# Optimization experiments

Measured on AMD Instinct MI355X. Metric: run time of the kernel, lower is better.

## Reference

```python
import jax, jax.numpy as jnp
import numpy as np

N, F_IN, F_OUT, K = 4096, 32, 32, 2
NEG_SLOPE = 0.2
MASK_VAL = -9e15


def _sparse_mat(kv, km, density=0.01):
    vals = jax.random.normal(kv, (N, N), dtype=jnp.float32)
    mask = jax.random.uniform(km, (N, N)) < density
    return vals * mask


def setup_inputs() -> dict:
    key = jax.random.key(0)
    ks = jax.random.split(key, 12)
    x = jax.random.normal(ks[0], (N, F_IN), dtype=jnp.float32)
    Ld = _sparse_mat(ks[1], ks[2])
    Lu = _sparse_mat(ks[3], ks[4])
    P = jax.random.normal(ks[5], (N, N), dtype=jnp.float32) / np.sqrt(N)
    W1 = jax.random.normal(ks[6], (K, F_IN, F_OUT), dtype=jnp.float32) * 0.1
    W2 = jax.random.normal(ks[7], (K, F_IN, F_OUT), dtype=jnp.float32) * 0.1
    W0 = jax.random.normal(ks[8], (F_IN, F_OUT), dtype=jnp.float32) * 0.1
    att1 = jax.random.normal(ks[9], (2 * F_OUT * K, 1), dtype=jnp.float32) * 0.1
    att2 = jax.random.normal(ks[10], (2 * F_OUT * K, 1), dtype=jnp.float32) * 0.1
    return {"x": x, "Ld": Ld, "Lu": Lu, "P": P, "W1": W1, "W2": W2,
            "W0": W0, "att1": att1, "att2": att2}


def _branch(x, L, W, att):
    # W: [K, F_in, F_out]; precompute x @ W[k] for all k -> [K, N, F_out]
    Kk, _, Fo = W.shape
    xw = jnp.einsum('nf,kfo->kno', x, W)
    # torch.cat([x@W[k]], dim=1) == transpose+reshape of xw
    xcat = jnp.transpose(xw, (1, 0, 2)).reshape(x.shape[0], Kk * Fo)
    d = Fo * Kk
    e = xcat @ att[:d] + (xcat @ att[d:]).T            # [N, N]
    e = jax.nn.leaky_relu(e, negative_slope=NEG_SLOPE)
    e = jnp.where(L != 0, e, MASK_VAL)
    alpha = jax.nn.softmax(e, axis=1)                   # row softmax, no dropout (eval)
    z = alpha @ xw[0]
    a = alpha
    for k in range(1, Kk):
        a = a @ L
        z = z + a @ xw[k]
    return z


def reference(x, Ld, Lu, P, W1, W2, W0, att1, att2):
    z1 = _branch(x, Ld, W1, att1)
    z2 = _branch(x, Lu, W2, att2)
    x0 = P @ (x @ W0)
    return z1 + z2 + x0
```

## Files before the change

kernel.cpp:

```cpp
#include <hip/hip_runtime.h>
#include <hip/hip_bf16.h>

#define NN 4096
#define CAP 128
#define KS 8

typedef __attribute__((ext_vector_type(8))) short bf16x8;
typedef __attribute__((ext_vector_type(4))) float f32x4;

__device__ __forceinline__ float lrelu(float v) { return v >= 0.f ? v : 0.2f * v; }

__device__ __forceinline__ ushort f2bu(float f) {
    unsigned u = __float_as_uint(f);
    return (ushort)((u + 0x7FFFu + ((u >> 16) & 1u)) >> 16);
}

__global__ __launch_bounds__(256) void k_prep(
    const float* __restrict__ x,
    const float* __restrict__ W1, const float* __restrict__ W2,
    const float* __restrict__ W0,
    const float* __restrict__ att1, const float* __restrict__ att2,
    float* __restrict__ xwA1, float* __restrict__ xwB1,
    float* __restrict__ xwA2, float* __restrict__ xwB2,
    float* __restrict__ a1, float* __restrict__ b1,
    float* __restrict__ a2, float* __restrict__ b2,
    __hip_bfloat16* __restrict__ Bt)
{
    __shared__ float wl[5120];
    __shared__ float xs[256];
    const int t = threadIdx.x;
    for (int i = t; i < 2048; i += 256) { wl[i] = W1[i]; wl[2048 + i] = W2[i]; }
    for (int i = t; i < 1024; i += 256) wl[4096 + i] = W0[i];
    const int rowBase = blockIdx.x * 8;
    xs[t] = x[rowBase * 32 + t];
    __syncthreads();

    const int o = t & 31, r = t >> 5;
    const int row = rowBase + r;
    const float* xr = &xs[r * 32];
    float vA1 = 0.f, vB1 = 0.f, vA2 = 0.f, vB2 = 0.f, v0 = 0.f;
#pragma unroll
    for (int f = 0; f < 32; ++f) {
        const float xv = xr[f];
        vA1 += xv * wl[f * 32 + o];
        vB1 += xv * wl[1024 + f * 32 + o];
        vA2 += xv * wl[2048 + f * 32 + o];
        vB2 += xv * wl[3072 + f * 32 + o];
        v0  += xv * wl[4096 + f * 32 + o];
    }
    xwA1[row * 32 + o] = vA1;
    xwB1[row * 32 + o] = vB1;
    xwA2[row * 32 + o] = vA2;
    xwB2[row * 32 + o] = vB2;
    ((ushort*)Bt)[(size_t)o * NN + row] = f2bu(v0);

    float pa1 = vA1 * att1[o]      + vB1 * att1[32 + o];
    float pb1 = vA1 * att1[64 + o] + vB1 * att1[96 + o];
    float pa2 = vA2 * att2[o]      + vB2 * att2[32 + o];
    float pb2 = vA2 * att2[64 + o] + vB2 * att2[96 + o];
#pragma unroll
    for (int m = 1; m <= 16; m <<= 1) {
        pa1 += __shfl_xor(pa1, m); pb1 += __shfl_xor(pb1, m);
        pa2 += __shfl_xor(pa2, m); pb2 += __shfl_xor(pb2, m);
    }
    if (o == 0) { a1[row] = pa1; b1[row] = pb1; a2[row] = pa2; b2[row] = pb2; }
}

__global__ __launch_bounds__(256) void k_csr(
    const float* __restrict__ Ld, const float* __restrict__ Lu,
    int2* __restrict__ csrv, int* __restrict__ cntArr)
{
    const int row = blockIdx.x;
    const int t = threadIdx.x, lane = t & 63, w = t >> 6;
    __shared__ int wcnt[16];

    float4 v[8];
    const float4* A4 = (const float4*)(Ld + (size_t)row * NN);
    const float4* B4 = (const float4*)(Lu + (size_t)row * NN);
#pragma unroll
    for (int it = 0; it < 4; ++it) { v[it] = A4[it * 256 + t]; v[4 + it] = B4[it * 256 + t]; }

    const unsigned long long lt = (1ull << lane) - 1ull;
#pragma unroll
    for (int br = 0; br < 2; ++br) {
        int2* out = csrv + ((size_t)br * NN + row) * CAP;
        int tots[4];
#pragma unroll
        for (int it = 0; it < 4; ++it) {
            const float4 fv = v[br * 4 + it];
            tots[it] = __popcll(__ballot(fv.x != 0.f)) + __popcll(__ballot(fv.y != 0.f))
                     + __popcll(__ballot(fv.z != 0.f)) + __popcll(__ballot(fv.w != 0.f));
        }
        __syncthreads();
        if (lane == 0) {
            int4 tv; tv.x = tots[0]; tv.y = tots[1]; tv.z = tots[2]; tv.w = tots[3];
            *(int4*)&wcnt[w * 4] = tv;
        }
        __syncthreads();
        const int4 ca = *(const int4*)&wcnt[0];
        const int4 cb = *(const int4*)&wcnt[4];
        const int4 cc = *(const int4*)&wcnt[8];
        const int4 cd = *(const int4*)&wcnt[12];
        const int cs[16] = {ca.x, ca.y, ca.z, ca.w, cb.x, cb.y, cb.z, cb.w,
                            cc.x, cc.y, cc.z, cc.w, cd.x, cd.y, cd.z, cd.w};
        int total = 0;
#pragma unroll
        for (int k2 = 0; k2 < 16; ++k2) total += cs[k2];
        int base = 0;
#pragma unroll
        for (int k2 = 0; k2 < 16; ++k2) base += (k2 < (w << 2)) ? cs[k2] : 0;
        const int cnt  = min(total, CAP);
        const int cp16 = min((cnt + 15) & ~15, CAP);

#pragma unroll
        for (int it = 0; it < 4; ++it) {
            const float4 fv = v[br * 4 + it];
            const unsigned long long m0 = __ballot(fv.x != 0.f);
            const unsigned long long m1 = __ballot(fv.y != 0.f);
            const unsigned long long m2 = __ballot(fv.z != 0.f);
            const unsigned long long m3 = __ballot(fv.w != 0.f);
            const int p0 = __popcll(m0), p1 = __popcll(m1), p2 = __popcll(m2);
            const int c0 = (it * 256 + t) * 4;
            int s;
            s = base + __popcll(m0 & lt);
            if (fv.x != 0.f && s < CAP) { int2 e; e.x = c0;     e.y = __float_as_int(fv.x); out[s] = e; }
            s = base + p0 + __popcll(m1 & lt);
            if (fv.y != 0.f && s < CAP) { int2 e; e.x = c0 + 1; e.y = __float_as_int(fv.y); out[s] = e; }
            s = base + p0 + p1 + __popcll(m2 & lt);
            if (fv.z != 0.f && s < CAP) { int2 e; e.x = c0 + 2; e.y = __float_as_int(fv.z); out[s] = e; }
            s = base + p0 + p1 + p2 + __popcll(m3 & lt);
            if (fv.w != 0.f && s < CAP) { int2 e; e.x = c0 + 3; e.y = __float_as_int(fv.w); out[s] = e; }
            base += p0 + p1 + p2 + __popcll(m3);
        }
        if (t >= cnt && t < cp16) { int2 e; e.x = 0; e.y = 0; out[t] = e; }
        if (t == 0) cntArr[br * NN + row] = cnt;
    }
}

__global__ __launch_bounds__(256) void k_gather(
    const int2* __restrict__ csrv, const int* __restrict__ cntArr,
    const float* __restrict__ xwB1, const float* __restrict__ xwB2,
    const float* __restrict__ xwA1, const float* __restrict__ xwA2,
    float* __restrict__ u1, float* __restrict__ u2)
{
    __shared__ int2 sle[4][CAP];
    const int w = threadIdx.x >> 6, lane = threadIdx.x & 63;
    const int row = blockIdx.x * 4 + w;
    const int br  = blockIdx.y;
    const float* xwB = br ? xwB2 : xwB1;
    const float* xwA = br ? xwA2 : xwA1;
    float* u = br ? u2 : u1;

    const int cnt  = cntArr[br * NN + row];
    const int cp16 = min((cnt + 15) & ~15, CAP);
    const int2* ci = csrv + ((size_t)br * NN + row) * CAP;
    int2* se = sle[w];
    if (lane < cp16)      se[lane]      = ci[lane];
    if (lane + 64 < cp16) se[lane + 64] = ci[lane + 64];

    const int o = lane & 31, g = lane >> 5;
    float acc = 0.f;
    const int nb = cp16 >> 3;
    for (int j = 0; j < nb; ++j) {
        float wv[4], xv[4];
#pragma unroll
        for (int q = 0; q < 4; ++q) {
            const int2 e = se[8 * j + 2 * q + g];
            wv[q] = __int_as_float(e.y);
            xv[q] = xwB[(size_t)e.x * 32 + o];
        }
#pragma unroll
        for (int q = 0; q < 4; ++q) acc += wv[q] * xv[q];
    }
    acc += __shfl_xor(acc, 32);
    if (lane < 32) u[(size_t)row * 32 + o] = acc + xwA[(size_t)row * 32 + o];
}

__global__ __launch_bounds__(256) void k_attn(
    const int2* __restrict__ csrv, const int* __restrict__ cntArr,
    const float* __restrict__ a1, const float* __restrict__ b1,
    const float* __restrict__ a2, const float* __restrict__ b2,
    const float* __restrict__ u1, const float* __restrict__ u2,
    float* __restrict__ z1, float* __restrict__ z2)
{
    const int br = blockIdx.y;
    const int* cntB = cntArr + br * NN;
    const float* aA = br ? a2 : a1;
    const float* bA = br ? b2 : b1;
    const float* U  = br ? u2 : u1;
    float* z = br ? z2 : z1;

    __shared__ float sw[4 * CAP];
    __shared__ int   sci[4 * CAP];
    const int w = threadIdx.x >> 6, lane = threadIdx.x & 63;
    const int row = blockIdx.x * 4 + w;
    const int cnt = cntB[row];
    const int cp16 = min((cnt + 15) & ~15, CAP);
    const float ai = aA[row];
    const int2* ci = csrv + ((size_t)br * NN + row) * CAP;
    float* swg = sw + w * CAP;
    int*   scg = sci + w * CAP;

    int id0 = 0, id1 = 0;
    if (lane < cp16)      id0 = ci[lane].x;
    if (lane + 64 < cp16) id1 = ci[lane + 64].x;
    float e0 = (lane < cnt)      ? lrelu(ai + bA[id0]) : -1e30f;
    float e1 = (lane + 64 < cnt) ? lrelu(ai + bA[id1]) : -1e30f;
    float lmax = fmaxf(e0, e1);
#pragma unroll
    for (int m = 1; m <= 32; m <<= 1) lmax = fmaxf(lmax, __shfl_xor(lmax, m));
    const float w0 = __expf(e0 - lmax), w1 = __expf(e1 - lmax);
    float ssum = w0 + w1;
#pragma unroll
    for (int m = 1; m <= 32; m <<= 1) ssum += __shfl_xor(ssum, m);
    swg[lane] = w0; swg[lane + 64] = w1;
    scg[lane] = id0; scg[lane + 64] = id1;

    const int o = lane & 31, h = lane >> 5;
    float acc = 0.f;
    const int nb = cp16 >> 3;
    if (cnt > 0) {
        float wgA[4], uvA[4];
#pragma unroll
        for (int q = 0; q < 4; ++q) {
            const int s = h + 2 * q;
            wgA[q] = swg[s];
            uvA[q] = U[(size_t)scg[s] * 32 + o];
        }
        for (int j = 1; j < nb; ++j) {
            float wgB[4], uvB[4];
#pragma unroll
            for (int q = 0; q < 4; ++q) {
                const int s = h + 8 * j + 2 * q;
                wgB[q] = swg[s];
                uvB[q] = U[(size_t)scg[s] * 32 + o];
            }
#pragma unroll
            for (int q = 0; q < 4; ++q) acc += wgA[q] * uvA[q];
#pragma unroll
            for (int q = 0; q < 4; ++q) { wgA[q] = wgB[q]; uvA[q] = uvB[q]; }
        }
#pragma unroll
        for (int q = 0; q < 4; ++q) acc += wgA[q] * uvA[q];
    }
    acc += __shfl_xor(acc, 32);
    if (lane < 32) z[(size_t)row * 32 + o] = (cnt > 0) ? acc / ssum : 0.f;
}

__global__ __launch_bounds__(256) void k_pgemm(
    const float* __restrict__ P, const ushort* __restrict__ Bt,
    float* __restrict__ partial)
{
    __shared__ ushort sA[2][16 * 64 * 8];
    __shared__ ushort sB[2][8 * 64 * 8];
    const int t = threadIdx.x;
    const int row0 = blockIdx.x * 64;
    const int ks = blockIdx.y;
    const float4*  P4  = (const float4*)P;
    const ushort4* Bt4 = (const ushort4*)Bt;

    const int lane = t & 63, w = t >> 6;

    f32x4 acc0 = {0.f, 0.f, 0.f, 0.f};
    f32x4 acc1 = {0.f, 0.f, 0.f, 0.f};

    auto stageA = [&](int c, int buf) {
        const int kc4 = (ks * 512 + c * 128) >> 2;
#pragma unroll
        for (int j = 0; j < 8; ++j) {
            const int i = t + 256 * j;
            const int row = i >> 5, q = i & 31;
            const float4 v = P4[(size_t)(row0 + row) * 1024 + kc4 + q];
            ushort4 u;
            u.x = f2bu(v.x); u.y = f2bu(v.y); u.z = f2bu(v.z); u.w = f2bu(v.w);
            const int wi = row >> 4, m = row & 15;
            const int kk = q >> 3, quad = (q >> 1) & 3, jj = q & 1;
            *(ushort4*)&sA[buf][(((wi * 4 + kk) * 64) + quad * 16 + m) * 8 + jj * 4] = u;
        }
    };
    auto stageB = [&](int c, int buf) {
        const int kc4 = (ks * 512 + c * 128) >> 2;
#pragma unroll
        for (int j = 0; j < 4; ++j) {
            const int i = t + 256 * j;
            const int o = i >> 5, q = i & 31;
            const ushort4 u = Bt4[(size_t)o * 1024 + kc4 + q];
            const int nt = o >> 4, n = o & 15;
            const int kk = q >> 3, quad = (q >> 1) & 3, jj = q & 1;
            *(ushort4*)&sB[buf][(((kk * 2 + nt) * 64) + quad * 16 + n) * 8 + jj * 4] = u;
        }
    };
    auto compute = [&](int buf) {
        const ushort* pa = &sA[buf][(w * 4) * 64 * 8 + lane * 8];
        const ushort* pb = &sB[buf][lane * 8];
#pragma unroll
        for (int kk = 0; kk < 4; ++kk) {
            const bf16x8 a  = *(const bf16x8*)(pa + kk * 512);
            const bf16x8 b0 = *(const bf16x8*)(pb + kk * 1024);
            const bf16x8 b1 = *(const bf16x8*)(pb + kk * 1024 + 512);
            acc0 = __builtin_amdgcn_mfma_f32_16x16x32_bf16(a, b0, acc0, 0, 0, 0);
            acc1 = __builtin_amdgcn_mfma_f32_16x16x32_bf16(a, b1, acc1, 0, 0, 0);
        }
    };

    stageA(0, 0); stageB(0, 0);
    __syncthreads();
    for (int c = 0; c < 4; ++c) {
        if (c < 3) { stageA(c + 1, (c + 1) & 1); stageB(c + 1, (c + 1) & 1); }
        compute(c & 1);
        __syncthreads();
    }

    const int m = lane & 15, quad = lane >> 4;
    float* out = partial + ((size_t)ks * NN + row0 + w * 16 + quad * 4) * 32;
#pragma unroll
    for (int r = 0; r < 4; ++r) {
        out[r * 32 + m]      = acc0[r];
        out[r * 32 + 16 + m] = acc1[r];
    }
}

__global__ __launch_bounds__(256) void k_combine(
    const float4* __restrict__ z1, const float4* __restrict__ z2,
    const float4* __restrict__ partial, float4* __restrict__ out)
{
    const int i = blockIdx.x * 256 + threadIdx.x;
    const float4 a = z1[i], b = z2[i];
    float rx = a.x + b.x, ry = a.y + b.y, rz = a.z + b.z, rw = a.w + b.w;
#pragma unroll
    for (int p = 0; p < KS; ++p) {
        const float4 c = partial[p * 32768 + i];
        rx += c.x; ry += c.y; rz += c.z; rw += c.w;
    }
    float4 rr; rr.x = rx; rr.y = ry; rr.z = rz; rr.w = rw;
    out[i] = rr;
}

extern "C" void kernel_launch(void* const* d_in, const int* in_sizes, int n_in,
                              void* d_out, int out_size, void* d_ws, size_t ws_size,
                              hipStream_t stream) {
    (void)in_sizes; (void)n_in; (void)out_size; (void)ws_size;
    const float* x    = (const float*)d_in[0];
    const float* Ld   = (const float*)d_in[1];
    const float* Lu   = (const float*)d_in[2];
    const float* P    = (const float*)d_in[3];
    const float* W1   = (const float*)d_in[4];
    const float* W2   = (const float*)d_in[5];
    const float* W0   = (const float*)d_in[6];
    const float* att1 = (const float*)d_in[7];
    const float* att2 = (const float*)d_in[8];

    float* ws = (float*)d_ws;
    float* xwA1 = ws;
    float* xwB1 = ws + 131072;
    float* xwA2 = ws + 262144;
    float* xwB2 = ws + 393216;
    float* u1   = ws + 524288;
    float* u2   = ws + 655360;
    float* z1   = ws + 786432;
    float* z2   = ws + 917504;
    float* a1   = ws + 1048576;
    float* b1   = ws + 1052672;
    float* a2   = ws + 1056768;
    float* b2   = ws + 1060864;
    float* partial = ws + 1064960;
    __hip_bfloat16* Bt = (__hip_bfloat16*)(ws + 2113536);
    int2* csrv = (int2*)(ws + 2179072);
    int*  cnt  = (int*)(ws + 4276224);

    k_prep<<<512, 256, 0, stream>>>(x, W1, W2, W0, att1, att2,
                                    xwA1, xwB1, xwA2, xwB2, a1, b1, a2, b2, Bt);
    k_csr<<<NN, 256, 0, stream>>>(Ld, Lu, csrv, cnt);
    k_gather<<<dim3(NN / 4, 2), 256, 0, stream>>>(csrv, cnt, xwB1, xwB2,
                                                  xwA1, xwA2, u1, u2);
    k_attn<<<dim3(NN / 4, 2), 256, 0, stream>>>(csrv, cnt, a1, b1, a2, b2,
                                                u1, u2, z1, z2);
    k_pgemm<<<dim3(64, KS), 256, 0, stream>>>(P, (const ushort*)Bt, partial);
    k_combine<<<128, 256, 0, stream>>>((const float4*)z1, (const float4*)z2,
                                       (const float4*)partial, (float4*)d_out);
}
```

Baseline: 235.9 us.

## Co-schedule P GEMM with CSR build and fuse combine into attention

The dense P@(xW0) GEMM blocks are interleaved into the CSR-extraction kernel (every 9th block does GEMM work), so the compute-bound MFMA work overlaps with the bandwidth-bound scan of Ld/Lu. The attention kernel now handles both branches per row and also sums the split-K partials, writing the final output directly. This removes the separate pgemm and combine launches and the z1/z2 round-trips. In exchange, the GEMM loses its double-buffered LDS staging, and the fused kernel's shared memory footprint may reduce occupancy for the CSR blocks.

```diff
diff --git a/kernel.cpp b/kernel.cpp
--- a/kernel.cpp
+++ b/kernel.cpp
@@ -66,74 +66,134 @@
     if (o == 0) { a1[row] = pa1; b1[row] = pb1; a2[row] = pa2; b2[row] = pb2; }
 }
 
-__global__ __launch_bounds__(256) void k_csr(
+__global__ __launch_bounds__(256) void k_work(
     const float* __restrict__ Ld, const float* __restrict__ Lu,
-    int2* __restrict__ csrv, int* __restrict__ cntArr)
+    const float* __restrict__ P, const ushort* __restrict__ Bt,
+    int2* __restrict__ csrv, int* __restrict__ cntArr,
+    float* __restrict__ partial)
 {
-    const int row = blockIdx.x;
-    const int t = threadIdx.x, lane = t & 63, w = t >> 6;
-    __shared__ int wcnt[16];
-
-    float4 v[8];
-    const float4* A4 = (const float4*)(Ld + (size_t)row * NN);
-    const float4* B4 = (const float4*)(Lu + (size_t)row * NN);
-#pragma unroll
-    for (int it = 0; it < 4; ++it) { v[it] = A4[it * 256 + t]; v[4 + it] = B4[it * 256 + t]; }
-
-    const unsigned long long lt = (1ull << lane) - 1ull;
-#pragma unroll
-    for (int br = 0; br < 2; ++br) {
-        int2* out = csrv + ((size_t)br * NN + row) * CAP;
-        int tots[4];
-#pragma unroll
-        for (int it = 0; it < 4; ++it) {
-            const float4 fv = v[br * 4 + it];
-            tots[it] = __popcll(__ballot(fv.x != 0.f)) + __popcll(__ballot(fv.y != 0.f))
-                     + __popcll(__ballot(fv.z != 0.f)) + __popcll(__ballot(fv.w != 0.f));
-        }
-        __syncthreads();
-        if (lane == 0) {
-            int4 tv; tv.x = tots[0]; tv.y = tots[1]; tv.z = tots[2]; tv.w = tots[3];
-            *(int4*)&wcnt[w * 4] = tv;
-        }
-        __syncthreads();
-        const int4 ca = *(const int4*)&wcnt[0];
-        const int4 cb = *(const int4*)&wcnt[4];
-        const int4 cc = *(const int4*)&wcnt[8];
-        const int4 cd = *(const int4*)&wcnt[12];
-        const int cs[16] = {ca.x, ca.y, ca.z, ca.w, cb.x, cb.y, cb.z, cb.w,
-                            cc.x, cc.y, cc.z, cc.w, cd.x, cd.y, cd.z, cd.w};
-        int total = 0;
-#pragma unroll
-        for (int k2 = 0; k2 < 16; ++k2) total += cs[k2];
-        int base = 0;
-#pragma unroll
-        for (int k2 = 0; k2 < 16; ++k2) base += (k2 < (w << 2)) ? cs[k2] : 0;
-        const int cnt  = min(total, CAP);
-        const int cp16 = min((cnt + 15) & ~15, CAP);
-
-#pragma unroll
-        for (int it = 0; it < 4; ++it) {
-            const float4 fv = v[br * 4 + it];
-            const unsigned long long m0 = __ballot(fv.x != 0.f);
-            const unsigned long long m1 = __ballot(fv.y != 0.f);
-            const unsigned long long m2 = __ballot(fv.z != 0.f);
-            const unsigned long long m3 = __ballot(fv.w != 0.f);
-            const int p0 = __popcll(m0), p1 = __popcll(m1), p2 = __popcll(m2);
-            const int c0 = (it * 256 + t) * 4;
-            int s;
-            s = base + __popcll(m0 & lt);
-            if (fv.x != 0.f && s < CAP) { int2 e; e.x = c0;     e.y = __float_as_int(fv.x); out[s] = e; }
-            s = base + p0 + __popcll(m1 & lt);
-            if (fv.y != 0.f && s < CAP) { int2 e; e.x = c0 + 1; e.y = __float_as_int(fv.y); out[s] = e; }
-            s = base + p0 + p1 + __popcll(m2 & lt);
-            if (fv.z != 0.f && s < CAP) { int2 e; e.x = c0 + 2; e.y = __float_as_int(fv.z); out[s] = e; }
-            s = base + p0 + p1 + p2 + __popcll(m3 & lt);
-            if (fv.w != 0.f && s < CAP) { int2 e; e.x = c0 + 3; e.y = __float_as_int(fv.w); out[s] = e; }
-            base += p0 + p1 + p2 + __popcll(m3);
-        }
-        if (t >= cnt && t < cp16) { int2 e; e.x = 0; e.y = 0; out[t] = e; }
-        if (t == 0) cntArr[br * NN + row] = cnt;
+    __shared__ ushort sA[16 * 64 * 8];
+    __shared__ ushort sB[8 * 64 * 8];
+    const int t = threadIdx.x;
+    const int lane = t & 63, w = t >> 6;
+    const int bx = blockIdx.x;
+
+    if (bx % 9 == 0) {
+        const int bp = bx / 9;
+        const int row0 = (bp & 63) * 64;
+        const int ks = bp >> 6;
+        const float4*  P4  = (const float4*)P;
+        const ushort4* Bt4 = (const ushort4*)Bt;
+        f32x4 acc0 = {0.f, 0.f, 0.f, 0.f};
+        f32x4 acc1 = {0.f, 0.f, 0.f, 0.f};
+
+        for (int c = 0; c < 4; ++c) {
+            const int kc4 = (ks * 512 + c * 128) >> 2;
+#pragma unroll
+            for (int j = 0; j < 8; ++j) {
+                const int i = t + 256 * j;
+                const int row = i >> 5, q = i & 31;
+                const float4 v = P4[(size_t)(row0 + row) * 1024 + kc4 + q];
+                ushort4 u;
+                u.x = f2bu(v.x); u.y = f2bu(v.y); u.z = f2bu(v.z); u.w = f2bu(v.w);
+                const int wi = row >> 4, m = row & 15;
+                const int kk = q >> 3, quad = (q >> 1) & 3, jj = q & 1;
+                *(ushort4*)&sA[(((wi * 4 + kk) * 64) + quad * 16 + m) * 8 + jj * 4] = u;
+            }
+#pragma unroll
+            for (int j = 0; j < 4; ++j) {
+                const int i = t + 256 * j;
+                const int o = i >> 5, q = i & 31;
+                const ushort4 u = Bt4[(size_t)o * 1024 + kc4 + q];
+                const int nt = o >> 4, n = o & 15;
+                const int kk = q >> 3, quad = (q >> 1) & 3, jj = q & 1;
+                *(ushort4*)&sB[(((kk * 2 + nt) * 64) + quad * 16 + n) * 8 + jj * 4] = u;
+            }
+            __syncthreads();
+            const ushort* pa = &sA[(w * 4) * 64 * 8 + lane * 8];
+            const ushort* pb = &sB[lane * 8];
+#pragma unroll
+            for (int kk = 0; kk < 4; ++kk) {
+                const bf16x8 a  = *(const bf16x8*)(pa + kk * 512);
+                const bf16x8 b0 = *(const bf16x8*)(pb + kk * 1024);
+                const bf16x8 b1 = *(const bf16x8*)(pb + kk * 1024 + 512);
+                acc0 = __builtin_amdgcn_mfma_f32_16x16x32_bf16(a, b0, acc0, 0, 0, 0);
+                acc1 = __builtin_amdgcn_mfma_f32_16x16x32_bf16(a, b1, acc1, 0, 0, 0);
+            }
+            __syncthreads();
+        }
+        const int m = lane & 15, quad = lane >> 4;
+        float* out = partial + ((size_t)ks * NN + row0 + w * 16 + quad * 4) * 32;
+#pragma unroll
+        for (int r = 0; r < 4; ++r) {
+            out[r * 32 + m]      = acc0[r];
+            out[r * 32 + 16 + m] = acc1[r];
+        }
+    } else {
+        const int row = bx - 1 - bx / 9;
+        int* wcnt = (int*)sA;
+
+        float4 v[8];
+        const float4* A4 = (const float4*)(Ld + (size_t)row * NN);
+        const float4* B4 = (const float4*)(Lu + (size_t)row * NN);
+#pragma unroll
+        for (int it = 0; it < 4; ++it) { v[it] = A4[it * 256 + t]; v[4 + it] = B4[it * 256 + t]; }
+
+        const unsigned long long lt = (1ull << lane) - 1ull;
+#pragma unroll
+        for (int br = 0; br < 2; ++br) {
+            int2* out = csrv + ((size_t)br * NN + row) * CAP;
+            int tots[4];
+#pragma unroll
+            for (int it = 0; it < 4; ++it) {
+                const float4 fv = v[br * 4 + it];
+                tots[it] = __popcll(__ballot(fv.x != 0.f)) + __popcll(__ballot(fv.y != 0.f))
+                         + __popcll(__ballot(fv.z != 0.f)) + __popcll(__ballot(fv.w != 0.f));
+            }
+            __syncthreads();
+            if (lane == 0) {
+                int4 tv; tv.x = tots[0]; tv.y = tots[1]; tv.z = tots[2]; tv.w = tots[3];
+                *(int4*)&wcnt[w * 4] = tv;
+            }
+            __syncthreads();
+            const int4 ca = *(const int4*)&wcnt[0];
+            const int4 cb = *(const int4*)&wcnt[4];
+            const int4 cc = *(const int4*)&wcnt[8];
+            const int4 cd = *(const int4*)&wcnt[12];
+            const int cs[16] = {ca.x, ca.y, ca.z, ca.w, cb.x, cb.y, cb.z, cb.w,
+                                cc.x, cc.y, cc.z, cc.w, cd.x, cd.y, cd.z, cd.w};
+            int total = 0;
+#pragma unroll
+            for (int k2 = 0; k2 < 16; ++k2) total += cs[k2];
+            int base = 0;
+#pragma unroll
+            for (int k2 = 0; k2 < 16; ++k2) base += (k2 < (w << 2)) ? cs[k2] : 0;
+            const int cnt  = min(total, CAP);
+            const int cp16 = min((cnt + 15) & ~15, CAP);
+
+#pragma unroll
+            for (int it = 0; it < 4; ++it) {
+                const float4 fv = v[br * 4 + it];
+                const unsigned long long m0 = __ballot(fv.x != 0.f);
+                const unsigned long long m1 = __ballot(fv.y != 0.f);
+                const unsigned long long m2 = __ballot(fv.z != 0.f);
+                const unsigned long long m3 = __ballot(fv.w != 0.f);
+                const int p0 = __popcll(m0), p1 = __popcll(m1), p2 = __popcll(m2);
+                const int c0 = (it * 256 + t) * 4;
+                int s;
+                s = base + __popcll(m0 & lt);
+                if (fv.x != 0.f && s < CAP) { int2 e; e.x = c0;     e.y = __float_as_int(fv.x); out[s] = e; }
+                s = base + p0 + __popcll(m1 & lt);
+                if (fv.y != 0.f && s < CAP) { int2 e; e.x = c0 + 1; e.y = __float_as_int(fv.y); out[s] = e; }
+                s = base + p0 + p1 + __popcll(m2 & lt);
+                if (fv.z != 0.f && s < CAP) { int2 e; e.x = c0 + 2; e.y = __float_as_int(fv.z); out[s] = e; }
+                s = base + p0 + p1 + p2 + __popcll(m3 & lt);
+                if (fv.w != 0.f && s < CAP) { int2 e; e.x = c0 + 3; e.y = __float_as_int(fv.w); out[s] = e; }
+                base += p0 + p1 + p2 + __popcll(m3);
+            }
+            if (t >= cnt && t < cp16) { int2 e; e.x = 0; e.y = 0; out[t] = e; }
+            if (t == 0) cntArr[br * NN + row] = cnt;
+        }
     }
 }
 
@@ -176,164 +236,83 @@
     if (lane < 32) u[(size_t)row * 32 + o] = acc + xwA[(size_t)row * 32 + o];
 }
 
-__global__ __launch_bounds__(256) void k_attn(
+__global__ __launch_bounds__(256) void k_attn2(
     const int2* __restrict__ csrv, const int* __restrict__ cntArr,
     const float* __restrict__ a1, const float* __restrict__ b1,
     const float* __restrict__ a2, const float* __restrict__ b2,
     const float* __restrict__ u1, const float* __restrict__ u2,
-    float* __restrict__ z1, float* __restrict__ z2)
+    const float* __restrict__ partial, float* __restrict__ outp)
 {
-    const int br = blockIdx.y;
-    const int* cntB = cntArr + br * NN;
-    const float* aA = br ? a2 : a1;
-    const float* bA = br ? b2 : b1;
-    const float* U  = br ? u2 : u1;
-    float* z = br ? z2 : z1;
-
     __shared__ float sw[4 * CAP];
     __shared__ int   sci[4 * CAP];
     const int w = threadIdx.x >> 6, lane = threadIdx.x & 63;
     const int row = blockIdx.x * 4 + w;
-    const int cnt = cntB[row];
-    const int cp16 = min((cnt + 15) & ~15, CAP);
-    const float ai = aA[row];
-    const int2* ci = csrv + ((size_t)br * NN + row) * CAP;
     float* swg = sw + w * CAP;
     int*   scg = sci + w * CAP;
-
-    int id0 = 0, id1 = 0;
-    if (lane < cp16)      id0 = ci[lane].x;
-    if (lane + 64 < cp16) id1 = ci[lane + 64].x;
-    float e0 = (lane < cnt)      ? lrelu(ai + bA[id0]) : -1e30f;
-    float e1 = (lane + 64 < cnt) ? lrelu(ai + bA[id1]) : -1e30f;
-    float lmax = fmaxf(e0, e1);
-#pragma unroll
-    for (int m = 1; m <= 32; m <<= 1) lmax = fmaxf(lmax, __shfl_xor(lmax, m));
-    const float w0 = __expf(e0 - lmax), w1 = __expf(e1 - lmax);
-    float ssum = w0 + w1;
-#pragma unroll
-    for (int m = 1; m <= 32; m <<= 1) ssum += __shfl_xor(ssum, m);
-    swg[lane] = w0; swg[lane + 64] = w1;
-    scg[lane] = id0; scg[lane + 64] = id1;
-
     const int o = lane & 31, h = lane >> 5;
-    float acc = 0.f;
-    const int nb = cp16 >> 3;
-    if (cnt > 0) {
-        float wgA[4], uvA[4];
-#pragma unroll
-        for (int q = 0; q < 4; ++q) {
-            const int s = h + 2 * q;
-            wgA[q] = swg[s];
-            uvA[q] = U[(size_t)scg[s] * 32 + o];
-        }
-        for (int j = 1; j < nb; ++j) {
-            float wgB[4], uvB[4];
+    float total = 0.f;
+
+#pragma unroll
+    for (int br = 0; br < 2; ++br) {
+        const float* aA = br ? a2 : a1;
+        const float* bA = br ? b2 : b1;
+        const float* U  = br ? u2 : u1;
+        const int cnt = cntArr[br * NN + row];
+        const int cp16 = min((cnt + 15) & ~15, CAP);
+        const float ai = aA[row];
+        const int2* ci = csrv + ((size_t)br * NN + row) * CAP;
+
+        int id0 = 0, id1 = 0;
+        if (lane < cp16)      id0 = ci[lane].x;
+        if (lane + 64 < cp16) id1 = ci[lane + 64].x;
+        float e0 = (lane < cnt)      ? lrelu(ai + bA[id0]) : -1e30f;
+        float e1 = (lane + 64 < cnt) ? lrelu(ai + bA[id1]) : -1e30f;
+        float lmax = fmaxf(e0, e1);
+#pragma unroll
+        for (int m = 1; m <= 32; m <<= 1) lmax = fmaxf(lmax, __shfl_xor(lmax, m));
+        const float w0 = __expf(e0 - lmax), w1 = __expf(e1 - lmax);
+        float ssum = w0 + w1;
+#pragma unroll
+        for (int m = 1; m <= 32; m <<= 1) ssum += __shfl_xor(ssum, m);
+        swg[lane] = w0; swg[lane + 64] = w1;
+        scg[lane] = id0; scg[lane + 64] = id1;
+
+        float acc = 0.f;
+        const int nb = cp16 >> 3;
+        if (cnt > 0) {
+            float wgA[4], uvA[4];
 #pragma unroll
             for (int q = 0; q < 4; ++q) {
-                const int s = h + 8 * j + 2 * q;
-                wgB[q] = swg[s];
-                uvB[q] = U[(size_t)scg[s] * 32 + o];
+                const int s = h + 2 * q;
+                wgA[q] = swg[s];
+                uvA[q] = U[(size_t)scg[s] * 32 + o];
+            }
+            for (int j = 1; j < nb; ++j) {
+                float wgB[4], uvB[4];
+#pragma unroll
+                for (int q = 0; q < 4; ++q) {
+                    const int s = h + 8 * j + 2 * q;
+                    wgB[q] = swg[s];
+                    uvB[q] = U[(size_t)scg[s] * 32 + o];
+                }
+#pragma unroll
+                for (int q = 0; q < 4; ++q) acc += wgA[q] * uvA[q];
+#pragma unroll
+                for (int q = 0; q < 4; ++q) { wgA[q] = wgB[q]; uvA[q] = uvB[q]; }
             }
 #pragma unroll
             for (int q = 0; q < 4; ++q) acc += wgA[q] * uvA[q];
-#pragma unroll
-            for (int q = 0; q < 4; ++q) { wgA[q] = wgB[q]; uvA[q] = uvB[q]; }
-        }
-#pragma unroll
-        for (int q = 0; q < 4; ++q) acc += wgA[q] * uvA[q];
-    }
-    acc += __shfl_xor(acc, 32);
-    if (lane < 32) z[(size_t)row * 32 + o] = (cnt > 0) ? acc / ssum : 0.f;
-}
-
-__global__ __launch_bounds__(256) void k_pgemm(
-    const float* __restrict__ P, const ushort* __restrict__ Bt,
-    float* __restrict__ partial)
-{
-    __shared__ ushort sA[2][16 * 64 * 8];
-    __shared__ ushort sB[2][8 * 64 * 8];
-    const int t = threadIdx.x;
-    const int row0 = blockIdx.x * 64;
-    const int ks = blockIdx.y;
-    const float4*  P4  = (const float4*)P;
-    const ushort4* Bt4 = (const ushort4*)Bt;
-
-    const int lane = t & 63, w = t >> 6;
-
-    f32x4 acc0 = {0.f, 0.f, 0.f, 0.f};
-    f32x4 acc1 = {0.f, 0.f, 0.f, 0.f};
-
-    auto stageA = [&](int c, int buf) {
-        const int kc4 = (ks * 512 + c * 128) >> 2;
-#pragma unroll
-        for (int j = 0; j < 8; ++j) {
-            const int i = t + 256 * j;
-            const int row = i >> 5, q = i & 31;
-            const float4 v = P4[(size_t)(row0 + row) * 1024 + kc4 + q];
-            ushort4 u;
-            u.x = f2bu(v.x); u.y = f2bu(v.y); u.z = f2bu(v.z); u.w = f2bu(v.w);
-            const int wi = row >> 4, m = row & 15;
-            const int kk = q >> 3, quad = (q >> 1) & 3, jj = q & 1;
-            *(ushort4*)&sA[buf][(((wi * 4 + kk) * 64) + quad * 16 + m) * 8 + jj * 4] = u;
-        }
-    };
-    auto stageB = [&](int c, int buf) {
-        const int kc4 = (ks * 512 + c * 128) >> 2;
-#pragma unroll
-        for (int j = 0; j < 4; ++j) {
-            const int i = t + 256 * j;
-            const int o = i >> 5, q = i & 31;
-            const ushort4 u = Bt4[(size_t)o * 1024 + kc4 + q];
-            const int nt = o >> 4, n = o & 15;
-            const int kk = q >> 3, quad = (q >> 1) & 3, jj = q & 1;
-            *(ushort4*)&sB[buf][(((kk * 2 + nt) * 64) + quad * 16 + n) * 8 + jj * 4] = u;
-        }
-    };
-    auto compute = [&](int buf) {
-        const ushort* pa = &sA[buf][(w * 4) * 64 * 8 + lane * 8];
-        const ushort* pb = &sB[buf][lane * 8];
-#pragma unroll
-        for (int kk = 0; kk < 4; ++kk) {
-            const bf16x8 a  = *(const bf16x8*)(pa + kk * 512);
-            const bf16x8 b0 = *(const bf16x8*)(pb + kk * 1024);
-            const bf16x8 b1 = *(const bf16x8*)(pb + kk * 1024 + 512);
-            acc0 = __builtin_amdgcn_mfma_f32_16x16x32_bf16(a, b0, acc0, 0, 0, 0);
-            acc1 = __builtin_amdgcn_mfma_f32_16x16x32_bf16(a, b1, acc1, 0, 0, 0);
-        }
-    };
-
-    stageA(0, 0); stageB(0, 0);
-    __syncthreads();
-    for (int c = 0; c < 4; ++c) {
-        if (c < 3) { stageA(c + 1, (c + 1) & 1); stageB(c + 1, (c + 1) & 1); }
-        compute(c & 1);
-        __syncthreads();
-    }
-
-    const int m = lane & 15, quad = lane >> 4;
-    float* out = partial + ((size_t)ks * NN + row0 + w * 16 + quad * 4) * 32;
-#pragma unroll
-    for (int r = 0; r < 4; ++r) {
-        out[r * 32 + m]      = acc0[r];
-        out[r * 32 + 16 + m] = acc1[r];
-    }
-}
-
-__global__ __launch_bounds__(256) void k_combine(
-    const float4* __restrict__ z1, const float4* __restrict__ z2,
-    const float4* __restrict__ partial, float4* __restrict__ out)
-{
-    const int i = blockIdx.x * 256 + threadIdx.x;
-    const float4 a = z1[i], b = z2[i];
-    float rx = a.x + b.x, ry = a.y + b.y, rz = a.z + b.z, rw = a.w + b.w;
-#pragma unroll
-    for (int p = 0; p < KS; ++p) {
-        const float4 c = partial[p * 32768 + i];
-        rx += c.x; ry += c.y; rz += c.z; rw += c.w;
-    }
-    float4 rr; rr.x = rx; rr.y = ry; rr.z = rz; rr.w = rw;
-    out[i] = rr;
+        }
+        acc += __shfl_xor(acc, 32);
+        if (cnt > 0) total += acc / ssum;
+    }
+
+    if (lane < 32) {
+#pragma unroll
+        for (int p = 0; p < KS; ++p)
+            total += partial[(size_t)p * NN * 32 + (size_t)row * 32 + o];
+        outp[(size_t)row * 32 + o] = total;
+    }
 }
 
 extern "C" void kernel_launch(void* const* d_in, const int* in_sizes, int n_in,
@@ -357,25 +336,21 @@
     float* xwB2 = ws + 393216;
     float* u1   = ws + 524288;
     float* u2   = ws + 655360;
-    float* z1   = ws + 786432;
-    float* z2   = ws + 917504;
-    float* a1   = ws + 1048576;
-    float* b1   = ws + 1052672;
-    float* a2   = ws + 1056768;
-    float* b2   = ws + 1060864;
-    float* partial = ws + 1064960;
-    __hip_bfloat16* Bt = (__hip_bfloat16*)(ws + 2113536);
-    int2* csrv = (int2*)(ws + 2179072);
-    int*  cnt  = (int*)(ws + 4276224);
+    float* a1   = ws + 786432;
+    float* b1   = ws + 790528;
+    float* a2   = ws + 794624;
+    float* b2   = ws + 798720;
+    float* partial = ws + 802816;
+    __hip_bfloat16* Bt = (__hip_bfloat16*)(ws + 1851392);
+    int2* csrv = (int2*)(ws + 1916928);
+    int*  cnt  = (int*)(ws + 4014080);
 
     k_prep<<<512, 256, 0, stream>>>(x, W1, W2, W0, att1, att2,
                                     xwA1, xwB1, xwA2, xwB2, a1, b1, a2, b2, Bt);
-    k_csr<<<NN, 256, 0, stream>>>(Ld, Lu, csrv, cnt);
+    k_work<<<4608, 256, 0, stream>>>(Ld, Lu, P, (const ushort*)Bt,
+                                     csrv, cnt, partial);
     k_gather<<<dim3(NN / 4, 2), 256, 0, stream>>>(csrv, cnt, xwB1, xwB2,
                                                   xwA1, xwA2, u1, u2);
-    k_attn<<<dim3(NN / 4, 2), 256, 0, stream>>>(csrv, cnt, a1, b1, a2, b2,
-                                                u1, u2, z1, z2);
-    k_pgemm<<<dim3(64, KS), 256, 0, stream>>>(P, (const ushort*)Bt, partial);
-    k_combine<<<128, 256, 0, stream>>>((const float4*)z1, (const float4*)z2,
-                                       (const float4*)partial, (float4*)d_out);
-}
+    k_attn2<<<NN / 4, 256, 0, stream>>>(csrv, cnt, a1, b1, a2, b2,
+                                        u1, u2, partial, (float*)d_out);
+}
```

Result: slower. 243.3 us (+3.1%).
